# Kernel optimization log

Measured on AMD Instinct MI355X. Metric: run time of the kernel, lower is better.

## Reference

```python
import jax, jax.numpy as jnp
import numpy as np

N = 50000   # nodes
E = 800000  # edges
C = 64      # node feature channels (0e)
A = 4       # edge attr channels
B = 16      # edge embedding (radial basis) size
H = 8       # radial MLP hidden size
D = 32      # query/key channels
P = 16      # node attr channels
R_MAX = 5.0


def setup_inputs() -> dict:
    key = jax.random.key(0)
    ks = jax.random.split(key, 20)
    w = lambda k, shape, fan_in: (jax.random.normal(k, shape, jnp.float32) / np.sqrt(fan_in).astype(np.float32))
    inp = {
        "node_feats": jax.random.normal(ks[0], (N, C), jnp.float32),
        "node_attrs": jax.random.normal(ks[1], (N, P), jnp.float32),
        "edge_embedding": jax.random.uniform(ks[2], (E, B), jnp.float32),
        "edge_attrs": jax.random.normal(ks[3], (E, A), jnp.float32),
        "positions": jax.random.normal(ks[4], (N, 3), jnp.float32) * 0.3,  # keep lengths < r_max
        "edge_src": jax.random.randint(ks[5], (E,), 0, N),
        "edge_dst": jax.random.randint(ks[6], (E,), 0, N),
        # parameters
        "W_q": w(ks[7], (C, D), C),            # h_q Linear
        "W1_k": w(ks[8], (B, H), B),           # radial MLP for tp_k
        "W2_k": w(ks[9], (H, C * A), H),
        "W1_v": w(ks[10], (B, H), B),          # radial MLP for tp_v
        "W2_v": w(ks[11], (H, C * A), H),
        "W_lin_k": w(ks[12], (C, D), C),       # linear_k
        "W_lin_v": w(ks[13], (C, C), C),       # linear_v
        "W_dot": w(ks[14], (D, D), D * D),     # FullyConnectedTensorProduct(q,k,'0e')
        "W_sc": w(ks[15], (C, P, C), C * P),   # self connection FCTP
    }
    return inp


def soft_unit_step(x):
    safe = jnp.where(x > 0, x, 1.0)
    return jnp.where(x > 0, jnp.exp(-1.0 / safe), 0.0)


def uvu_tp(x_src, edge_attrs, edge_embedding, W1, W2):
    # radial MLP -> per-edge, per-path weights [E, C, A]; 'uvu' tensor product on scalars
    wgt = (jax.nn.silu(edge_embedding @ W1) @ W2).reshape(-1, C, A)
    return x_src * (jnp.einsum('eca,ea->ec', wgt, edge_attrs) / np.sqrt(A).astype(np.float32))


def reference(node_feats, node_attrs, edge_embedding, edge_attrs, positions,
              edge_src, edge_dst, W_q, W1_k, W2_k, W1_v, W2_v,
              W_lin_k, W_lin_v, W_dot, W_sc):
    q = (node_feats @ W_q)[edge_dst]                              # [E, D]
    x_src = node_feats[edge_src]                                  # [E, C]
    k = uvu_tp(x_src, edge_attrs, edge_embedding, W1_k, W2_k) @ W_lin_k  # [E, D]
    v = uvu_tp(x_src, edge_attrs, edge_embedding, W1_v, W2_v) @ W_lin_v  # [E, C]

    edge_vec = positions[edge_dst] - positions[edge_src]
    edge_length = jnp.linalg.norm(edge_vec, axis=1)               # [E]
    cutoff = soft_unit_step(2.0 * R_MAX * (1.0 - edge_length / R_MAX))

    score = jnp.einsum('ei,ij,ej->e', q, W_dot, k)                # weighted bilinear dot -> 0e
    expv = cutoff * jnp.exp(score)                                # [E]
    z = jax.ops.segment_sum(expv, edge_dst, num_segments=N)       # softmax normalizer
    z = jnp.where(z == 0, 1.0, z)
    alpha = expv / z[edge_dst]
    msg = jnp.sqrt(jax.nn.relu(alpha))[:, None] * v               # [E, C]
    node_out = jax.ops.segment_sum(msg, edge_dst, num_segments=N)  # [N, C]

    sc = jnp.einsum('nc,np,cpo->no', node_feats, node_attrs, W_sc)
    return node_out + sc
```

## Files before the change

### kernel.cpp

```cpp
#include <hip/hip_runtime.h>
#include <math.h>

#define NN 50000
#define EE 800000
#define NPAD 50176
#define CPAD 68

typedef __attribute__((ext_vector_type(8))) short short8v;
typedef __attribute__((ext_vector_type(4))) float f32x4;

static __device__ __forceinline__ short bf16r(float x) {
  union { float f; unsigned u; } v; v.f = x;
  unsigned r = v.u + 0x7FFFu + ((v.u >> 16) & 1u);
  return (short)(r >> 16);
}
static __device__ __forceinline__ float bf2f(unsigned u) {
  union { unsigned u; float f; } v; v.u = u << 16;
  return v.f;
}
static __device__ __forceinline__ unsigned pk2(float a, float b) {
  return (unsigned)(unsigned short)bf16r(a) | ((unsigned)(unsigned short)bf16r(b) << 16);
}


__global__ __launch_bounds__(256) void fold_kernel(
    const float* __restrict__ Wq, const float* __restrict__ Wdot,
    const float* __restrict__ Wlk, const float* __restrict__ W2k,
    const float* __restrict__ W2v, const float* __restrict__ Wlv,
    float* __restrict__ M, unsigned short* __restrict__ w2kT,
    unsigned short* __restrict__ w2vT, unsigned short* __restrict__ wlvb)
{
  __shared__ float tmp[2048];
  const int tid = threadIdx.x;
#pragma unroll
  for (int r = 0; r < 8; ++r) {
    int idx = tid + r * 256;
    int cin = idx >> 5, d = idx & 31;
    float a = 0.f;
    for (int j = 0; j < 32; ++j) a = fmaf(Wq[cin * 32 + j], Wdot[j * 32 + d], a);
    tmp[idx] = a;
  }
  __syncthreads();
#pragma unroll
  for (int r = 0; r < 16; ++r) {
    int idx = tid + r * 256;
    int cin = idx >> 6, c = idx & 63;
    float a = 0.f;
    for (int d = 0; d < 32; ++d) a = fmaf(tmp[cin * 32 + d], Wlk[c * 32 + d], a);
    M[idx] = a;
  }
#pragma unroll
  for (int r = 0; r < 8; ++r) {
    int idx = tid + r * 256;
    int c = idx >> 5, k = idx & 31, h = k >> 2, a = k & 3;
    w2kT[idx] = (unsigned short)bf16r(W2k[h * 256 + c * 4 + a]);
    w2vT[idx] = (unsigned short)bf16r(W2v[h * 256 + c * 4 + a]);
  }
#pragma unroll
  for (int r = 0; r < 16; ++r) {
    int idx = tid + r * 256;
    int o = idx >> 6, c = idx & 63;
    wlvb[idx] = (unsigned short)bf16r(Wlv[c * 64 + o]);
  }
}

__global__ __launch_bounds__(256) void prep_wsc(
    const float* __restrict__ Wsc, unsigned short* __restrict__ wscb)
{
  int w = blockIdx.x * 256 + threadIdx.x;
  int c = w & 63, o = (w >> 6) & 63, p = w >> 12;
  wscb[w] = (unsigned short)bf16r(Wsc[c * 1024 + p * 64 + o]);
}

__global__ __launch_bounds__(256) void hist_kernel(
    const int* __restrict__ edst, int* __restrict__ cur)
{
  int e = blockIdx.x * 256 + threadIdx.x;
  atomicAdd(&cur[edst[e]], 1);
}

__global__ __launch_bounds__(256) void scanA_kernel(
    int* __restrict__ cur, int* __restrict__ bsum)
{
  __shared__ int s[256];
  const int tid = threadIdx.x;
  const int i = blockIdx.x * 256 + tid;
  int v = cur[i];
  s[tid] = v;
  __syncthreads();
  for (int off = 1; off < 256; off <<= 1) {
    int t = (tid >= off) ? s[tid - off] : 0;
    __syncthreads();
    s[tid] += t;
    __syncthreads();
  }
  cur[i] = s[tid] - v;
  if (tid == 255) bsum[blockIdx.x] = s[255];
}

__global__ __launch_bounds__(256) void scanB_kernel(int* __restrict__ bsum)
{
  __shared__ int s[256];
  const int tid = threadIdx.x;
  int v = (tid < 196) ? bsum[tid] : 0;
  s[tid] = v;
  __syncthreads();
  for (int off = 1; off < 256; off <<= 1) {
    int t = (tid >= off) ? s[tid - off] : 0;
    __syncthreads();
    s[tid] += t;
    __syncthreads();
  }
  if (tid < 196) bsum[tid] = s[tid] - v;
}

__global__ __launch_bounds__(256) void scanC_kernel(
    int* __restrict__ cur, const int* __restrict__ bsum)
{
  const int i = blockIdx.x * 256 + threadIdx.x;
  cur[i] += bsum[blockIdx.x];
}

__global__ __launch_bounds__(256) void scatter_fused(
    const int* __restrict__ esrc, const int* __restrict__ edst,
    const float* __restrict__ ea, const float* __restrict__ eb,
    const float* __restrict__ pos, const float* __restrict__ W1k,
    const float* __restrict__ W1v, int* __restrict__ cur,
    int* __restrict__ perm, float* __restrict__ rec)
{
  int e = blockIdx.x * 256 + threadIdx.x;
  int s = esrc[e], d = edst[e];
  int r = atomicAdd(&cur[d], 1);
  perm[r] = e;
  float dx = pos[d * 3 + 0] - pos[s * 3 + 0];
  float dy = pos[d * 3 + 1] - pos[s * 3 + 1];
  float dz = pos[d * 3 + 2] - pos[s * 3 + 2];
  float len = sqrtf(fmaf(dx, dx, fmaf(dy, dy, dz * dz)));
  float arg = 10.f - 2.f * len;
  float cl = (arg > 0.f) ? __expf(-1.f / arg) : 0.f;
  const f32x4* eb4 = reinterpret_cast<const f32x4*>(eb);
  f32x4 q0 = eb4[e * 4 + 0], q1 = eb4[e * 4 + 1],
        q2 = eb4[e * 4 + 2], q3 = eb4[e * 4 + 3];
  float ebv[16] = {q0.x, q0.y, q0.z, q0.w, q1.x, q1.y, q1.z, q1.w,
                   q2.x, q2.y, q2.z, q2.w, q3.x, q3.y, q3.z, q3.w};
  float h[16];
#pragma unroll
  for (int j = 0; j < 16; ++j) h[j] = 0.f;
#pragma unroll
  for (int b = 0; b < 16; ++b) {
    float x = ebv[b];
#pragma unroll
    for (int j = 0; j < 8; ++j) {
      h[j]     = fmaf(x, W1k[b * 8 + j], h[j]);
      h[8 + j] = fmaf(x, W1v[b * 8 + j], h[8 + j]);
    }
  }
#pragma unroll
  for (int j = 0; j < 16; ++j) h[j] = h[j] / (1.f + __expf(-h[j]));

  f32x4 a4 = reinterpret_cast<const f32x4*>(ea)[e];
  f32x4* rp4 = reinterpret_cast<f32x4*>(rec + (size_t)e * 12);
  f32x4 w0, w1, w2;
  w0.x = cl;
  w0.y = __uint_as_float(pk2(a4.x, a4.y));
  w0.z = __uint_as_float(pk2(a4.z, a4.w));
  w0.w = 0.f;
  w1.x = __uint_as_float(pk2(h[0], h[1]));
  w1.y = __uint_as_float(pk2(h[2], h[3]));
  w1.z = __uint_as_float(pk2(h[4], h[5]));
  w1.w = __uint_as_float(pk2(h[6], h[7]));
  w2.x = __uint_as_float(pk2(h[8], h[9]));
  w2.y = __uint_as_float(pk2(h[10], h[11]));
  w2.z = __uint_as_float(pk2(h[12], h[13]));
  w2.w = __uint_as_float(pk2(h[14], h[15]));
  rp4[0] = w0;
  rp4[1] = w1;
  rp4[2] = w2;
}

__global__ __launch_bounds__(256) void tq_kernel(
    const float* __restrict__ nf, const float* __restrict__ M, float* __restrict__ tq)
{
  __shared__ float Ml[4096];
  __shared__ float nfl[64 * 68];
  const int tid = threadIdx.x;
  const int base = blockIdx.x * 64;
#pragma unroll
  for (int r = 0; r < 4; ++r) {
    int idx = tid + r * 256;
    reinterpret_cast<float4*>(Ml)[idx] = reinterpret_cast<const float4*>(M)[idx];
  }
#pragma unroll
  for (int r = 0; r < 4; ++r) {
    int idx = tid + r * 256;
    int row = idx >> 4, c4 = idx & 15;
    float4 v = make_float4(0.f, 0.f, 0.f, 0.f);
    if (base + row < NN) v = reinterpret_cast<const float4*>(nf)[(base + row) * 16 + c4];
    *reinterpret_cast<float4*>(&nfl[row * 68 + c4 * 4]) = v;
  }
  __syncthreads();
  const int to = tid & 15, tn = tid >> 4;
  float4 acc[4] = {make_float4(0,0,0,0), make_float4(0,0,0,0),
                   make_float4(0,0,0,0), make_float4(0,0,0,0)};
  for (int c = 0; c < 64; ++c) {
    float4 m = reinterpret_cast<const float4*>(Ml)[c * 16 + to];
#pragma unroll
    for (int i = 0; i < 4; ++i) {
      float x = nfl[(tn * 4 + i) * 68 + c];
      acc[i].x = fmaf(x, m.x, acc[i].x);
      acc[i].y = fmaf(x, m.y, acc[i].y);
      acc[i].z = fmaf(x, m.z, acc[i].z);
      acc[i].w = fmaf(x, m.w, acc[i].w);
    }
  }
#pragma unroll
  for (int i = 0; i < 4; ++i) {
    int n = base + tn * 4 + i;
    if (n < NN) reinterpret_cast<float4*>(tq)[n * 16 + to] = acc[i];
  }
}

__global__ __launch_bounds__(256) void edge_kernel(
    const float* __restrict__ nf, const float* __restrict__ tq,
    const float* __restrict__ rec, const int* __restrict__ perm,
    const int* __restrict__ esrc, const int* __restrict__ edst,
    const unsigned short* __restrict__ w2kT, const unsigned short* __restrict__ w2vT,
    float* __restrict__ z, float* __restrict__ U)
{
  __shared__ float xs[64 * CPAD];
  __shared__ int   es[64];
  __shared__ int   ed[64];
  __shared__ float cl[64];
  __shared__ float evs[64];
  const int tid  = threadIdx.x;
  const int lane = tid & 63;
  const int lo = lane & 15, hi = lane >> 4;
  const int w = tid >> 6;
  const int sb = blockIdx.x * 64;
  const int row = 16 * w + lo;

  short8v bk[4], bv[4];
#pragma unroll
  for (int t = 0; t < 4; ++t) {
    bk[t] = *reinterpret_cast<const short8v*>(&w2kT[(16 * t + lo) * 32 + hi * 8]);
    bv[t] = *reinterpret_cast<const short8v*>(&w2vT[(16 * t + lo) * 32 + hi * 8]);
  }
  const int eL = perm[sb + row];
  if (tid < 64) {
    int pe = perm[sb + tid];
    es[tid] = esrc[pe];
    ed[tid] = edst[pe];
    cl[tid] = rec[(size_t)pe * 12];
  }
  const unsigned* ru = reinterpret_cast<const unsigned*>(rec);
  const size_t rb = (size_t)eL * 12;
  unsigned ea01 = ru[rb + 1];
  unsigned ea23 = ru[rb + 2];
  unsigned k01 = ru[rb + 4 + hi];
  unsigned v01 = ru[rb + 8 + hi];

  __syncthreads();

#pragma unroll
  for (int r = 0; r < 4; ++r) {
    int idx = tid + r * 256;
    int e = idx >> 4, c4 = idx & 15;
    float4 xv = reinterpret_cast<const float4*>(nf)[es[e] * 16 + c4];
    *reinterpret_cast<float4*>(&xs[e * CPAD + c4 * 4]) = xv;
  }

  float ax = bf2f(ea01 & 0xffffu), ay = bf2f(ea01 >> 16);
  float az = bf2f(ea23 & 0xffffu), aw = bf2f(ea23 >> 16);
  float hk0 = bf2f(k01 & 0xffffu), hk1 = bf2f(k01 >> 16);
  float hv0 = bf2f(v01 & 0xffffu), hv1 = bf2f(v01 >> 16);
  short8v ak, av;
  ak[0] = bf16r(hk0 * ax); ak[1] = bf16r(hk0 * ay);
  ak[2] = bf16r(hk0 * az); ak[3] = bf16r(hk0 * aw);
  ak[4] = bf16r(hk1 * ax); ak[5] = bf16r(hk1 * ay);
  ak[6] = bf16r(hk1 * az); ak[7] = bf16r(hk1 * aw);
  av[0] = bf16r(hv0 * ax); av[1] = bf16r(hv0 * ay);
  av[2] = bf16r(hv0 * az); av[3] = bf16r(hv0 * aw);
  av[4] = bf16r(hv1 * ax); av[5] = bf16r(hv1 * ay);
  av[6] = bf16r(hv1 * az); av[7] = bf16r(hv1 * aw);

  __syncthreads();

  f32x4 zero = {0.f, 0.f, 0.f, 0.f};
  f32x4 ack[4], acv[4];
#pragma unroll
  for (int t = 0; t < 4; ++t) {
    ack[t] = __builtin_amdgcn_mfma_f32_16x16x32_bf16(ak, bk[t], zero, 0, 0, 0);
    acv[t] = __builtin_amdgcn_mfma_f32_16x16x32_bf16(av, bv[t], zero, 0, 0, 0);
  }

  const int erow = 16 * w + 4 * hi;
  float p0, p1, p2, p3;
  {
    const float* x0 = &xs[(erow + 0) * CPAD + lo];
    const float* x1 = &xs[(erow + 1) * CPAD + lo];
    const float* x2 = &xs[(erow + 2) * CPAD + lo];
    const float* x3 = &xs[(erow + 3) * CPAD + lo];
    const float* t0 = tq + (size_t)ed[erow + 0] * 64 + lo;
    const float* t1 = tq + (size_t)ed[erow + 1] * 64 + lo;
    const float* t2 = tq + (size_t)ed[erow + 2] * 64 + lo;
    const float* t3 = tq + (size_t)ed[erow + 3] * 64 + lo;
    p0 = (x0[0]*t0[0])*ack[0][0] + (x0[16]*t0[16])*ack[1][0] + (x0[32]*t0[32])*ack[2][0] + (x0[48]*t0[48])*ack[3][0];
    p1 = (x1[0]*t1[0])*ack[0][1] + (x1[16]*t1[16])*ack[1][1] + (x1[32]*t1[32])*ack[2][1] + (x1[48]*t1[48])*ack[3][1];
    p2 = (x2[0]*t2[0])*ack[0][2] + (x2[16]*t2[16])*ack[1][2] + (x2[32]*t2[32])*ack[2][2] + (x2[48]*t2[48])*ack[3][2];
    p3 = (x3[0]*t3[0])*ack[0][3] + (x3[16]*t3[16])*ack[1][3] + (x3[32]*t3[32])*ack[2][3] + (x3[48]*t3[48])*ack[3][3];
  }
#pragma unroll
  for (int off = 1; off < 16; off <<= 1) {
    p0 += __shfl_xor(p0, off);
    p1 += __shfl_xor(p1, off);
    p2 += __shfl_xor(p2, off);
    p3 += __shfl_xor(p3, off);
  }
  float ev0 = cl[erow + 0] * __expf(0.5f * p0);
  float ev1 = cl[erow + 1] * __expf(0.5f * p1);
  float ev2 = cl[erow + 2] * __expf(0.5f * p2);
  float ev3 = cl[erow + 3] * __expf(0.5f * p3);
  float se0 = sqrtf(ev0), se1 = sqrtf(ev1), se2 = sqrtf(ev2), se3 = sqrtf(ev3);
  if (lo < 4) {
    float ev = (lo == 0) ? ev0 : (lo == 1) ? ev1 : (lo == 2) ? ev2 : ev3;
    evs[erow + lo] = ev;
  }
#pragma unroll
  for (int i = 0; i < 4; ++i) {
    const float se = (i == 0) ? se0 : (i == 1) ? se1 : (i == 2) ? se2 : se3;
    float* xr = &xs[(erow + i) * CPAD + lo];
#pragma unroll
    for (int t = 0; t < 4; ++t) {
      xr[16 * t] = se * xr[16 * t] * acv[t][i];
    }
  }
  {
    const int c = lane;
    float acc = 0.f, evacc = 0.f;
    int prev = ed[16 * w];
    for (int r = 16 * w; r < 16 * w + 16; ++r) {
      int d = ed[r];
      if (d != prev) {
        unsafeAtomicAdd(&U[prev * 64 + c], acc);
        if (c == 0) unsafeAtomicAdd(&z[prev], evacc);
        acc = 0.f; evacc = 0.f; prev = d;
      }
      acc += xs[r * CPAD + c];
      if (c == 0) evacc += evs[r];
    }
    unsafeAtomicAdd(&U[prev * 64 + c], acc);
    if (c == 0) unsafeAtomicAdd(&z[prev], evacc);
  }
}

__global__ __launch_bounds__(256, 4) void final_kernel(
    const float* __restrict__ nf, const float* __restrict__ na,
    const float* __restrict__ U, const float* __restrict__ z,
    const unsigned short* __restrict__ wscb, const unsigned short* __restrict__ wlvb,
    float* __restrict__ out)
{
  __shared__ float nfl[64 * 68];
  __shared__ float Ul[64 * 68];
  __shared__ float nal[64 * 17];
  __shared__ float sl[64];
  const int tid = threadIdx.x;
  const int lane = tid & 63;
  const int lo = lane & 15, hi = lane >> 4;
  const int w = tid >> 6;
  const int nb = blockIdx.x * 64;

#pragma unroll
  for (int r = 0; r < 4; ++r) {
    int idx = tid + r * 256;
    int row = idx >> 4, c4 = idx & 15;
    int n = nb + row; if (n >= NN) n = NN - 1;
    float4 v = reinterpret_cast<const float4*>(nf)[n * 16 + c4];
    *reinterpret_cast<float4*>(&nfl[row * 68 + c4 * 4]) = v;
    float4 u = reinterpret_cast<const float4*>(U)[n * 16 + c4];
    *reinterpret_cast<float4*>(&Ul[row * 68 + c4 * 4]) = u;
  }
#pragma unroll
  for (int r = 0; r < 4; ++r) {
    int idx = tid + r * 256;
    int row = idx >> 4, p = idx & 15;
    int n = nb + row; if (n >= NN) n = NN - 1;
    nal[row * 17 + p] = na[n * 16 + p];
  }
  if (tid < 64) {
    int n = nb + tid; if (n >= NN) n = NN - 1;
    float zz = z[n];
    sl[tid] = (zz > 0.f) ? 0.5f * rsqrtf(zz) : 0.f;
  }
  __syncthreads();

  const int row = 16 * w + lo;
  short8v anf[2], au[2];
#pragma unroll
  for (int kk = 0; kk < 2; ++kk) {
#pragma unroll
    for (int j = 0; j < 8; ++j) {
      anf[kk][j] = bf16r(nfl[row * 68 + 32 * kk + 8 * hi + j]);
      au[kk][j]  = bf16r(Ul[row * 68 + 32 * kk + 8 * hi + j]);
    }
  }

  f32x4 zeroA = {0.f, 0.f, 0.f, 0.f};
  f32x4 accS[4] = {zeroA, zeroA, zeroA, zeroA};
  f32x4 accU[4] = {zeroA, zeroA, zeroA, zeroA};

#pragma unroll
  for (int t = 0; t < 4; ++t) {
    short8v b0 = *reinterpret_cast<const short8v*>(&wlvb[(16 * t + lo) * 64 + 8 * hi]);
    short8v b1 = *reinterpret_cast<const short8v*>(&wlvb[(16 * t + lo) * 64 + 32 + 8 * hi]);
    accU[t] = __builtin_amdgcn_mfma_f32_16x16x32_bf16(au[0], b0, accU[t], 0, 0, 0);
    accU[t] = __builtin_amdgcn_mfma_f32_16x16x32_bf16(au[1], b1, accU[t], 0, 0, 0);
  }
#pragma unroll 1
  for (int p = 0; p < 16; ++p) {
    f32x4 cp[4] = {zeroA, zeroA, zeroA, zeroA};
#pragma unroll
    for (int t = 0; t < 4; ++t) {
      const int bbase = (p * 64 + 16 * t + lo) * 64 + 8 * hi;
      short8v b0 = *reinterpret_cast<const short8v*>(&wscb[bbase]);
      short8v b1 = *reinterpret_cast<const short8v*>(&wscb[bbase + 32]);
      cp[t] = __builtin_amdgcn_mfma_f32_16x16x32_bf16(anf[0], b0, cp[t], 0, 0, 0);
      cp[t] = __builtin_amdgcn_mfma_f32_16x16x32_bf16(anf[1], b1, cp[t], 0, 0, 0);
    }
#pragma unroll
    for (int i = 0; i < 4; ++i) {
      float nav = nal[(16 * w + 4 * hi + i) * 17 + p];
#pragma unroll
      for (int t = 0; t < 4; ++t) accS[t][i] = fmaf(nav, cp[t][i], accS[t][i]);
    }
  }
#pragma unroll
  for (int i = 0; i < 4; ++i) {
    int n = nb + 16 * w + 4 * hi + i;
    if (n < NN) {
      float s = sl[16 * w + 4 * hi + i];
#pragma unroll
      for (int t = 0; t < 4; ++t) {
        out[n * 64 + 16 * t + lo] = fmaf(s, accU[t][i], accS[t][i]);
      }
    }
  }
}

extern "C" void kernel_launch(void* const* d_in, const int* in_sizes, int n_in,
                              void* d_out, int out_size, void* d_ws, size_t ws_size,
                              hipStream_t stream) {
  const float* nf   = (const float*)d_in[0];
  const float* na   = (const float*)d_in[1];
  const float* eb   = (const float*)d_in[2];
  const float* ea   = (const float*)d_in[3];
  const float* pos  = (const float*)d_in[4];
  const int*   esrc = (const int*)d_in[5];
  const int*   edst = (const int*)d_in[6];
  const float* Wq   = (const float*)d_in[7];
  const float* W1k  = (const float*)d_in[8];
  const float* W2k  = (const float*)d_in[9];
  const float* W1v  = (const float*)d_in[10];
  const float* W2v  = (const float*)d_in[11];
  const float* Wlk  = (const float*)d_in[12];
  const float* Wlv  = (const float*)d_in[13];
  const float* Wdot = (const float*)d_in[14];
  const float* Wsc  = (const float*)d_in[15];
  float* out = (float*)d_out;

  float* wsf = (float*)d_ws;
  float* z    = wsf;
  float* U    = wsf + 50176;
  int*   cur  = (int*)(wsf + 50176);
  int*   bsum = (int*)(wsf + 100352);
  float* M    = wsf + 100608;
  float* tq   = wsf + 3250176;
  unsigned short* wscb = (unsigned short*)(wsf + 3250176);
  unsigned short* w2kT = (unsigned short*)(wsf + 6450176);
  unsigned short* w2vT = (unsigned short*)(wsf + 6451200);
  unsigned short* wlvb = (unsigned short*)(wsf + 6452224);
  float* rec  = wsf + 6454272;
  int*   perm = (int*)(wsf + 16054272);

  fold_kernel<<<1, 256, 0, stream>>>(Wq, Wdot, Wlk, W2k, W2v, Wlv, M, w2kT, w2vT, wlvb);
  tq_kernel<<<(NN + 63) / 64, 256, 0, stream>>>(nf, M, tq);
  hipMemsetAsync(cur, 0, (size_t)(NPAD + 256) * sizeof(int), stream);
  hist_kernel<<<EE / 256, 256, 0, stream>>>(edst, cur);
  scanA_kernel<<<NPAD / 256, 256, 0, stream>>>(cur, bsum);
  scanB_kernel<<<1, 256, 0, stream>>>(bsum);
  scanC_kernel<<<NPAD / 256, 256, 0, stream>>>(cur, bsum);
  scatter_fused<<<EE / 256, 256, 0, stream>>>(esrc, edst, ea, eb, pos, W1k, W1v,
                                              cur, perm, rec);
  hipMemsetAsync(z, 0, (size_t)3250176 * sizeof(float), stream);
  edge_kernel<<<EE / 64, 256, 0, stream>>>(nf, tq, rec, perm, esrc, edst,
                                           w2kT, w2vT, z, U);
  prep_wsc<<<256, 256, 0, stream>>>(Wsc, wscb);
  final_kernel<<<(NN + 63) / 64, 256, 0, stream>>>(nf, na, U, z, wscb, wlvb, out);
}
```

Measured before the change: 322.7 us.

## Fuse prep kernels, fold memsets into histogram, drop scanC, use per-wave edge tiles

Merges the weight folding, Wsc conversion and counter zeroing into one multi-block prep kernel. Zeroing of z/U moves into the histogram kernel, and the scanC pass is removed by adding the block offset inside the scatter. The edge kernel now gives each wave its own 16-edge tile with wave barriers instead of block-wide __syncthreads. Together these remove several launches, memsets and block-level syncs, at the cost of a workspace layout reshuffle and an extra bsum load per edge.

```diff
diff --git a/kernel.cpp b/kernel.cpp
--- a/kernel.cpp
+++ b/kernel.cpp
@@ -4,7 +4,6 @@
 #define NN 50000
 #define EE 800000
 #define NPAD 50176
-#define CPAD 68
 
 typedef __attribute__((ext_vector_type(8))) short short8v;
 typedef __attribute__((ext_vector_type(4))) float f32x4;
@@ -23,60 +22,66 @@
 }
 
 
-__global__ __launch_bounds__(256) void fold_kernel(
+__global__ __launch_bounds__(256) void prep_kernel(
     const float* __restrict__ Wq, const float* __restrict__ Wdot,
     const float* __restrict__ Wlk, const float* __restrict__ W2k,
     const float* __restrict__ W2v, const float* __restrict__ Wlv,
-    float* __restrict__ M, unsigned short* __restrict__ w2kT,
-    unsigned short* __restrict__ w2vT, unsigned short* __restrict__ wlvb)
-{
-  __shared__ float tmp[2048];
+    const float* __restrict__ Wsc, float* __restrict__ M,
+    unsigned short* __restrict__ w2kT, unsigned short* __restrict__ w2vT,
+    unsigned short* __restrict__ wlvb, unsigned short* __restrict__ wscb,
+    int* __restrict__ cur)
+{
   const int tid = threadIdx.x;
-#pragma unroll
-  for (int r = 0; r < 8; ++r) {
-    int idx = tid + r * 256;
-    int cin = idx >> 5, d = idx & 31;
-    float a = 0.f;
-    for (int j = 0; j < 32; ++j) a = fmaf(Wq[cin * 32 + j], Wdot[j * 32 + d], a);
-    tmp[idx] = a;
-  }
-  __syncthreads();
-#pragma unroll
-  for (int r = 0; r < 16; ++r) {
-    int idx = tid + r * 256;
-    int cin = idx >> 6, c = idx & 63;
-    float a = 0.f;
-    for (int d = 0; d < 32; ++d) a = fmaf(tmp[cin * 32 + d], Wlk[c * 32 + d], a);
-    M[idx] = a;
-  }
-#pragma unroll
-  for (int r = 0; r < 8; ++r) {
-    int idx = tid + r * 256;
-    int c = idx >> 5, k = idx & 31, h = k >> 2, a = k & 3;
-    w2kT[idx] = (unsigned short)bf16r(W2k[h * 256 + c * 4 + a]);
-    w2vT[idx] = (unsigned short)bf16r(W2v[h * 256 + c * 4 + a]);
-  }
-#pragma unroll
-  for (int r = 0; r < 16; ++r) {
-    int idx = tid + r * 256;
-    int o = idx >> 6, c = idx & 63;
-    wlvb[idx] = (unsigned short)bf16r(Wlv[c * 64 + o]);
-  }
-}
-
-__global__ __launch_bounds__(256) void prep_wsc(
-    const float* __restrict__ Wsc, unsigned short* __restrict__ wscb)
-{
-  int w = blockIdx.x * 256 + threadIdx.x;
-  int c = w & 63, o = (w >> 6) & 63, p = w >> 12;
-  wscb[w] = (unsigned short)bf16r(Wsc[c * 1024 + p * 64 + o]);
-}
-
-__global__ __launch_bounds__(256) void hist_kernel(
-    const int* __restrict__ edst, int* __restrict__ cur)
-{
-  int e = blockIdx.x * 256 + threadIdx.x;
-  atomicAdd(&cur[edst[e]], 1);
+  const int b = blockIdx.x;
+  if (b == 0) {
+    __shared__ float tmp[2048];
+#pragma unroll
+    for (int r = 0; r < 8; ++r) {
+      int idx = tid + r * 256;
+      int cin = idx >> 5, d = idx & 31;
+      float a = 0.f;
+      for (int j = 0; j < 32; ++j) a = fmaf(Wq[cin * 32 + j], Wdot[j * 32 + d], a);
+      tmp[idx] = a;
+    }
+    __syncthreads();
+#pragma unroll
+    for (int r = 0; r < 16; ++r) {
+      int idx = tid + r * 256;
+      int cin = idx >> 6, c = idx & 63;
+      float a = 0.f;
+      for (int d = 0; d < 32; ++d) a = fmaf(tmp[cin * 32 + d], Wlk[c * 32 + d], a);
+      M[idx] = a;
+    }
+#pragma unroll
+    for (int r = 0; r < 8; ++r) {
+      int idx = tid + r * 256;
+      int c = idx >> 5, k = idx & 31, h = k >> 2, a = k & 3;
+      w2kT[idx] = (unsigned short)bf16r(W2k[h * 256 + c * 4 + a]);
+      w2vT[idx] = (unsigned short)bf16r(W2v[h * 256 + c * 4 + a]);
+    }
+#pragma unroll
+    for (int r = 0; r < 16; ++r) {
+      int idx = tid + r * 256;
+      int o = idx >> 6, c = idx & 63;
+      wlvb[idx] = (unsigned short)bf16r(Wlv[c * 64 + o]);
+    }
+  } else if (b <= 196) {
+    cur[(b - 1) * 256 + tid] = 0;
+  } else {
+    int w = (b - 197) * 256 + tid;
+    int c = w & 63, o = (w >> 6) & 63, p = w >> 12;
+    wscb[w] = (unsigned short)bf16r(Wsc[c * 1024 + p * 64 + o]);
+  }
+}
+
+__global__ __launch_bounds__(256) void hist_zero(
+    const int* __restrict__ edst, int* __restrict__ cur, float4* __restrict__ zu)
+{
+  int i = blockIdx.x * 256 + threadIdx.x;
+  float4 zf = make_float4(0.f, 0.f, 0.f, 0.f);
+  zu[i] = zf;
+  if (i < 12544) zu[800000 + i] = zf;
+  atomicAdd(&cur[edst[i]], 1);
 }
 
 __global__ __launch_bounds__(256) void scanA_kernel(
@@ -114,23 +119,17 @@
   if (tid < 196) bsum[tid] = s[tid] - v;
 }
 
-__global__ __launch_bounds__(256) void scanC_kernel(
-    int* __restrict__ cur, const int* __restrict__ bsum)
-{
-  const int i = blockIdx.x * 256 + threadIdx.x;
-  cur[i] += bsum[blockIdx.x];
-}
-
 __global__ __launch_bounds__(256) void scatter_fused(
     const int* __restrict__ esrc, const int* __restrict__ edst,
     const float* __restrict__ ea, const float* __restrict__ eb,
     const float* __restrict__ pos, const float* __restrict__ W1k,
     const float* __restrict__ W1v, int* __restrict__ cur,
-    int* __restrict__ perm, float* __restrict__ rec)
+    const int* __restrict__ bsum, int* __restrict__ perm,
+    float* __restrict__ rec)
 {
   int e = blockIdx.x * 256 + threadIdx.x;
   int s = esrc[e], d = edst[e];
-  int r = atomicAdd(&cur[d], 1);
+  int r = atomicAdd(&cur[d], 1) + bsum[d >> 8];
   perm[r] = e;
   float dx = pos[d * 3 + 0] - pos[s * 3 + 0];
   float dy = pos[d * 3 + 1] - pos[s * 3 + 1];
@@ -227,17 +226,21 @@
     const unsigned short* __restrict__ w2kT, const unsigned short* __restrict__ w2vT,
     float* __restrict__ z, float* __restrict__ U)
 {
-  __shared__ float xs[64 * CPAD];
-  __shared__ int   es[64];
-  __shared__ int   ed[64];
-  __shared__ float cl[64];
-  __shared__ float evs[64];
+  __shared__ float xsAll[4][16 * 68];
+  __shared__ int   esAll[4][16];
+  __shared__ int   edAll[4][16];
+  __shared__ float clAll[4][16];
+  __shared__ float evAll[4][16];
   const int tid  = threadIdx.x;
   const int lane = tid & 63;
+  const int w = tid >> 6;
   const int lo = lane & 15, hi = lane >> 4;
-  const int w = tid >> 6;
-  const int sb = blockIdx.x * 64;
-  const int row = 16 * w + lo;
+  const int sb = (blockIdx.x * 4 + w) * 16;
+  float* xs = xsAll[w];
+  int*   es = esAll[w];
+  int*   ed = edAll[w];
+  float* cl = clAll[w];
+  float* evs = evAll[w];
 
   short8v bk[4], bv[4];
 #pragma unroll
@@ -245,28 +248,28 @@
     bk[t] = *reinterpret_cast<const short8v*>(&w2kT[(16 * t + lo) * 32 + hi * 8]);
     bv[t] = *reinterpret_cast<const short8v*>(&w2vT[(16 * t + lo) * 32 + hi * 8]);
   }
-  const int eL = perm[sb + row];
-  if (tid < 64) {
-    int pe = perm[sb + tid];
-    es[tid] = esrc[pe];
-    ed[tid] = edst[pe];
-    cl[tid] = rec[(size_t)pe * 12];
-  }
+
+  const int eL = perm[sb + lo];
   const unsigned* ru = reinterpret_cast<const unsigned*>(rec);
   const size_t rb = (size_t)eL * 12;
   unsigned ea01 = ru[rb + 1];
   unsigned ea23 = ru[rb + 2];
-  unsigned k01 = ru[rb + 4 + hi];
-  unsigned v01 = ru[rb + 8 + hi];
-
-  __syncthreads();
+  unsigned k01  = ru[rb + 4 + hi];
+  unsigned v01  = ru[rb + 8 + hi];
+
+  if (hi == 0) {
+    es[lo] = esrc[eL];
+    ed[lo] = edst[eL];
+    cl[lo] = rec[rb];
+  }
+  __builtin_amdgcn_wave_barrier();
 
 #pragma unroll
   for (int r = 0; r < 4; ++r) {
-    int idx = tid + r * 256;
+    int idx = lane + r * 64;
     int e = idx >> 4, c4 = idx & 15;
     float4 xv = reinterpret_cast<const float4*>(nf)[es[e] * 16 + c4];
-    *reinterpret_cast<float4*>(&xs[e * CPAD + c4 * 4]) = xv;
+    *reinterpret_cast<float4*>(&xs[e * 68 + c4 * 4]) = xv;
   }
 
   float ax = bf2f(ea01 & 0xffffu), ay = bf2f(ea01 >> 16);
@@ -282,8 +285,7 @@
   av[2] = bf16r(hv0 * az); av[3] = bf16r(hv0 * aw);
   av[4] = bf16r(hv1 * ax); av[5] = bf16r(hv1 * ay);
   av[6] = bf16r(hv1 * az); av[7] = bf16r(hv1 * aw);
-
-  __syncthreads();
+  __builtin_amdgcn_wave_barrier();
 
   f32x4 zero = {0.f, 0.f, 0.f, 0.f};
   f32x4 ack[4], acv[4];
@@ -293,13 +295,13 @@
     acv[t] = __builtin_amdgcn_mfma_f32_16x16x32_bf16(av, bv[t], zero, 0, 0, 0);
   }
 
-  const int erow = 16 * w + 4 * hi;
+  const int erow = 4 * hi;
   float p0, p1, p2, p3;
   {
-    const float* x0 = &xs[(erow + 0) * CPAD + lo];
-    const float* x1 = &xs[(erow + 1) * CPAD + lo];
-    const float* x2 = &xs[(erow + 2) * CPAD + lo];
-    const float* x3 = &xs[(erow + 3) * CPAD + lo];
+    const float* x0 = &xs[(erow + 0) * 68 + lo];
+    const float* x1 = &xs[(erow + 1) * 68 + lo];
+    const float* x2 = &xs[(erow + 2) * 68 + lo];
+    const float* x3 = &xs[(erow + 3) * 68 + lo];
     const float* t0 = tq + (size_t)ed[erow + 0] * 64 + lo;
     const float* t1 = tq + (size_t)ed[erow + 1] * 64 + lo;
     const float* t2 = tq + (size_t)ed[erow + 2] * 64 + lo;
@@ -328,24 +330,26 @@
 #pragma unroll
   for (int i = 0; i < 4; ++i) {
     const float se = (i == 0) ? se0 : (i == 1) ? se1 : (i == 2) ? se2 : se3;
-    float* xr = &xs[(erow + i) * CPAD + lo];
+    float* xr = &xs[(erow + i) * 68 + lo];
 #pragma unroll
     for (int t = 0; t < 4; ++t) {
       xr[16 * t] = se * xr[16 * t] * acv[t][i];
     }
   }
+  __builtin_amdgcn_wave_barrier();
   {
     const int c = lane;
     float acc = 0.f, evacc = 0.f;
-    int prev = ed[16 * w];
-    for (int r = 16 * w; r < 16 * w + 16; ++r) {
+    int prev = ed[0];
+#pragma unroll
+    for (int r = 0; r < 16; ++r) {
       int d = ed[r];
       if (d != prev) {
         unsafeAtomicAdd(&U[prev * 64 + c], acc);
         if (c == 0) unsafeAtomicAdd(&z[prev], evacc);
         acc = 0.f; evacc = 0.f; prev = d;
       }
-      acc += xs[r * CPAD + c];
+      acc += xs[r * 68 + c];
       if (c == 0) evacc += evs[r];
     }
     unsafeAtomicAdd(&U[prev * 64 + c], acc);
@@ -470,29 +474,26 @@
   float* wsf = (float*)d_ws;
   float* z    = wsf;
   float* U    = wsf + 50176;
-  int*   cur  = (int*)(wsf + 50176);
-  int*   bsum = (int*)(wsf + 100352);
-  float* M    = wsf + 100608;
   float* tq   = wsf + 3250176;
-  unsigned short* wscb = (unsigned short*)(wsf + 3250176);
   unsigned short* w2kT = (unsigned short*)(wsf + 6450176);
   unsigned short* w2vT = (unsigned short*)(wsf + 6451200);
   unsigned short* wlvb = (unsigned short*)(wsf + 6452224);
-  float* rec  = wsf + 6454272;
-  int*   perm = (int*)(wsf + 16054272);
-
-  fold_kernel<<<1, 256, 0, stream>>>(Wq, Wdot, Wlk, W2k, W2v, Wlv, M, w2kT, w2vT, wlvb);
+  unsigned short* wscb = (unsigned short*)(wsf + 6454272);
+  int*   cur  = (int*)(wsf + 6487040);
+  int*   bsum = (int*)(wsf + 6537216);
+  float* M    = wsf + 6537472;
+  float* rec  = wsf + 6541568;
+  int*   perm = (int*)(wsf + 16141568);
+
+  prep_kernel<<<453, 256, 0, stream>>>(Wq, Wdot, Wlk, W2k, W2v, Wlv, Wsc,
+                                       M, w2kT, w2vT, wlvb, wscb, cur);
   tq_kernel<<<(NN + 63) / 64, 256, 0, stream>>>(nf, M, tq);
-  hipMemsetAsync(cur, 0, (size_t)(NPAD + 256) * sizeof(int), stream);
-  hist_kernel<<<EE / 256, 256, 0, stream>>>(edst, cur);
+  hist_zero<<<EE / 256, 256, 0, stream>>>(edst, cur, (float4*)z);
   scanA_kernel<<<NPAD / 256, 256, 0, stream>>>(cur, bsum);
   scanB_kernel<<<1, 256, 0, stream>>>(bsum);
-  scanC_kernel<<<NPAD / 256, 256, 0, stream>>>(cur, bsum);
   scatter_fused<<<EE / 256, 256, 0, stream>>>(esrc, edst, ea, eb, pos, W1k, W1v,
-                                              cur, perm, rec);
-  hipMemsetAsync(z, 0, (size_t)3250176 * sizeof(float), stream);
+                                              cur, bsum, perm, rec);
   edge_kernel<<<EE / 64, 256, 0, stream>>>(nf, tq, rec, perm, esrc, edst,
                                            w2kT, w2vT, z, U);
-  prep_wsc<<<256, 256, 0, stream>>>(Wsc, wscb);
   final_kernel<<<(NN + 63) / 64, 256, 0, stream>>>(nf, na, U, z, wscb, wlvb, out);
 }
```

Measured after the change: 303.6 us. 5.9% less time.
